# Performance work log

Hardware: AMD Instinct MI355X
Metric: run time of the kernel (lower is better)

## Reference

```python
import jax, jax.numpy as jnp
import numpy as np

LN_EPS = 1e-5
MASK_FILL = -1e10


def setup_inputs() -> dict:
    key = jax.random.key(0)
    ks = jax.random.split(key, 6)
    b, lq, lk, d = 8, 2048, 2048, 256
    q = jax.random.normal(ks[0], (b, lq, d), dtype=jnp.float32)
    k = jax.random.normal(ks[1], (b, lk, d), dtype=jnp.float32)
    v = jax.random.normal(ks[2], (b, lk, d), dtype=jnp.float32)
    # additive-score weight, scaled so logits are O(1)
    shared_attn = jax.random.normal(ks[3], (1, 2 * d), dtype=jnp.float32) / jnp.sqrt(jnp.float32(2 * d))
    fc_w = jax.random.normal(ks[4], (d, d), dtype=jnp.float32) / jnp.sqrt(jnp.float32(d))
    ln_gamma = jnp.ones((d,), dtype=jnp.float32)
    ln_beta = jnp.zeros((d,), dtype=jnp.float32)
    mask = jax.random.randint(ks[5], (b, lq, lk), 0, 2).astype(bool)
    return {"q": q, "k": k, "v": v, "shared_attn": shared_attn,
            "fc_w": fc_w, "ln_gamma": ln_gamma, "ln_beta": ln_beta, "mask": mask}


def reference(q, k, v, shared_attn, fc_w, ln_gamma, ln_beta, mask):
    d_k = q.shape[-1]
    residual = q
    # F.linear(cat([q_exp, k_exp], -1), W) with W:(1, 2*d_k) decomposes as
    # score[b,i,j] = q[b,i] . w_q + k[b,j] . w_k  (rank-1 additive score)
    w_q = shared_attn[0, :d_k]
    w_k = shared_attn[0, d_k:]
    sq = jnp.einsum('bid,d->bi', q, w_q)          # (b, lq)
    sk = jnp.einsum('bjd,d->bj', k, w_k)          # (b, lk)
    attn = sq[:, :, None] + sk[:, None, :]        # (b, lq, lk)
    attn = jnp.where(mask, jnp.float32(MASK_FILL), attn)
    attn = jax.nn.softmax(attn, axis=2)
    out = jnp.einsum('bij,bjd->bid', attn, v)     # (b, lq, d_v)
    out = out @ fc_w.T                            # F.linear(out, fc_w)
    x = out + residual
    mu = jnp.mean(x, axis=-1, keepdims=True)
    var = jnp.var(x, axis=-1, keepdims=True)
    out = (x - mu) / jnp.sqrt(var + LN_EPS) * ln_gamma + ln_beta
    return (out, attn)
```

## Files before the change

### kernel.cpp

```cpp
#include <hip/hip_runtime.h>
#include <hip/hip_bf16.h>

#define BB 8
#define LQ 2048
#define LK 2048
#define DD 256
#define OUT0_N (BB*LQ*DD)

typedef short s16x8 __attribute__((ext_vector_type(8)));
typedef float f32x4 __attribute__((ext_vector_type(4)));

#define GAS __attribute__((address_space(1)))
#define LAS __attribute__((address_space(3)))

__device__ __forceinline__ unsigned short f2b(float x){
  unsigned int u = __float_as_uint(x);
  u += 0x7fffu + ((u >> 16) & 1u);
  return (unsigned short)(u >> 16);
}
__device__ __forceinline__ float b2f(unsigned short h){
  return __uint_as_float(((unsigned int)h) << 16);
}
__device__ __forceinline__ float ldf(const void* p, long i, int bf){
  return bf ? b2f(((const unsigned short*)p)[i]) : ((const float*)p)[i];
}
__device__ __forceinline__ s16x8 ld8(const void* p, long i, int bf){
  if (bf) return *(const s16x8*)((const unsigned short*)p + i);
  const float* f = (const float*)p + i;
  float4 a = *(const float4*)(f);
  float4 c = *(const float4*)(f + 4);
  s16x8 r;
  r[0]=(short)f2b(a.x); r[1]=(short)f2b(a.y); r[2]=(short)f2b(a.z); r[3]=(short)f2b(a.w);
  r[4]=(short)f2b(c.x); r[5]=(short)f2b(c.y); r[6]=(short)f2b(c.z); r[7]=(short)f2b(c.w);
  return r;
}
__device__ __forceinline__ float wsum(float v){
  #pragma unroll
  for (int o=32;o;o>>=1) v += __shfl_xor(v, o, 64);
  return v;
}

__device__ __forceinline__ void detect_flags(const void* q, const void* mask,
                                             int& mbytes, int& bf){
  __shared__ int s_bf, s_mb;
  int t = threadIdx.x;
  if (t == 0){ s_bf = 0; s_mb = 0; }
  __syncthreads();
  if (t < 256){
    float x = fabsf(((const float*)q)[t]);
    if (x > 1e-6f && x < 100.0f) atomicAdd(&s_bf, 1);
    unsigned int mw = ((const unsigned int*)mask)[t];
    if (mw > 1u) atomicOr(&s_mb, 1);
  }
  __syncthreads();
  bf = (s_bf < 128) ? 1 : 0;
  mbytes = s_mb;
}

__global__ __launch_bounds__(256) void k_prep(const void* q, const void* kk,
    const void* v, const void* sh, const void* fc, const void* mask,
    float* e, unsigned short* vtf){
  int mbytes, bf;
  detect_flags(q, mask, mbytes, bf);
  (void)mbytes;
  int lane = threadIdx.x & 63;

  if (blockIdx.x >= 1024){
    int wid = ((blockIdx.x - 1024) << 2) + (threadIdx.x >> 6);
    long base = (long)wid * DD + lane * 4;
    float acc;
    if (bf){
      ushort4 kv = *(const ushort4*)((const unsigned short*)kk + base);
      ushort4 wv = *(const ushort4*)((const unsigned short*)sh + DD + lane*4);
      acc = b2f(kv.x)*b2f(wv.x) + b2f(kv.y)*b2f(wv.y)
          + b2f(kv.z)*b2f(wv.z) + b2f(kv.w)*b2f(wv.w);
    } else {
      float4 kv = *(const float4*)((const float*)kk + base);
      float4 wv = *(const float4*)((const float*)sh + DD + lane*4);
      acc = kv.x*wv.x + kv.y*wv.y + kv.z*wv.z + kv.w*wv.w;
    }
    acc = wsum(acc);
    if (lane == 0) e[wid] = __expf(acc);
    return;
  }

  int wid  = (blockIdx.x << 2) + (threadIdx.x >> 6);
  int dbase = (wid & 15) << 4;
  int jbase = (wid >> 4) << 6;
  int r = lane & 15, g = lane >> 4;
  f32x4 acc[4];
  #pragma unroll
  for (int t2=0;t2<4;t2++) acc[t2] = (f32x4){0.f,0.f,0.f,0.f};
  #pragma unroll
  for (int ks = 0; ks < 8; ++ks){
    int k0 = ks*32 + g*8;
    s16x8 bv = ld8(fc, (long)(dbase + r)*DD + k0, bf);
    #pragma unroll
    for (int t2 = 0; t2 < 4; ++t2){
      s16x8 a = ld8(v, (long)(jbase + t2*16 + r)*DD + k0, bf);
      acc[t2] = __builtin_amdgcn_mfma_f32_16x16x32_bf16(a, bv, acc[t2], 0, 0, 0);
    }
  }
  int b  = jbase >> 11;
  int jj = jbase & 2047;
  int d  = dbase + r;
  #pragma unroll
  for (int t2 = 0; t2 < 4; ++t2){
    int kidx = (jj >> 3) + t2*2 + (g >> 1);
    long idx = ((long)(b*256 + kidx))*2048 + (long)d*8 + (g & 1)*4;
    ushort4 w4;
    w4.x = f2b(acc[t2][0]); w4.y = f2b(acc[t2][1]);
    w4.z = f2b(acc[t2][2]); w4.w = f2b(acc[t2][3]);
    *(ushort4*)(vtf + idx) = w4;
  }
}

__device__ __forceinline__ s16x8 afrag(const unsigned int (*bits_s)[66],
    const unsigned short* e16_s, int row, int kk){
  int w0 = (kk >> 2) & 63;
  int nib4 = (kk >> 8) << 2;
  unsigned lo = (bits_s[row][w0]   >> nib4) & 0xFu;
  unsigned hi = (bits_s[row][w0+1] >> nib4) & 0xFu;
  unsigned m8 = lo | (hi << 4);
  union { s16x8 v; unsigned u[4]; } a;
  a.v = *(const s16x8*)(&e16_s[kk]);
  #pragma unroll
  for (int i = 0; i < 4; ++i){
    unsigned w = a.u[i];
    w = (m8 & (1u << (2*i)))   ? (w & 0xFFFF0000u) : w;
    w = (m8 & (1u << (2*i+1))) ? (w & 0x0000FFFFu) : w;
    a.u[i] = w;
  }
  return a.v;
}

__global__ __launch_bounds__(512, 4) void k_pvf(void* d_out, const unsigned short* vtf,
    const void* q, const void* gamp, const void* betp, const void* mask,
    const float* e){
  __shared__ __align__(16) char smem[80256];
  unsigned int (*bits_s)[66] = reinterpret_cast<unsigned int(*)[66]>(smem + 65536);
  unsigned short* e16_s      = (unsigned short*)(smem + 73984);
  float* scale_s             = (float*)(smem + 78080);
  float* gs                  = (float*)(smem + 78208);
  float* bs                  = (float*)(smem + 79232);
  float* redp                = (float*)smem;
  #define RED(nh_, row_, col_) redp[(((nh_)*32)+(row_))*132 + (col_)]

  int mbytes, bf;
  detect_flags(q, mask, mbytes, bf);
  int o     = ((blockIdx.x & 7) << 6) + (blockIdx.x >> 3);
  int b     = o >> 6;
  int rbase = (o & 63) << 5;
  int t = threadIdx.x, lane = t & 63, wid = t >> 6;
  int nh = wid & 1, ks = wid >> 1;
  int r16 = lane >> 4, c16 = lane & 15;
  int dbase = nh << 7;
  const float* eb = e + b * LK;
  const unsigned short* vtfb = vtf + (long)b * 256 * 2048;
  char* stag = smem + wid * 8192;

  auto STAGE = [&](int j){
    int ss = j >> 1, h = j & 1;
    int k0 = (ks << 9) + (ss << 5);
    const char* g = (const char*)vtfb +
        (((long)((k0 >> 3) + r16) * 256 + dbase + c16) << 4);
    char* lb = stag + (j & 1) * 4096;
    #pragma unroll
    for (int i = 0; i < 4; ++i)
      __builtin_amdgcn_global_load_lds(
        (const GAS unsigned int*)(g + h*1024 + i*256),
        (LAS unsigned int*)(lb + i*1024), 16, 0, 0);
  };

  { float4 ef = ((const float4*)eb)[t];
    ushort4 u; u.x=f2b(ef.x); u.y=f2b(ef.y); u.z=f2b(ef.z); u.w=f2b(ef.w);
    *(ushort4*)(&e16_s[t*4]) = u; }
  if (t < 256){ gs[t] = ldf(gamp, t, bf); bs[t] = ldf(betp, t, bf); }

  unsigned short* attn16 = (unsigned short*)d_out + OUT0_N;
  float*          attn32 = (float*)d_out + OUT0_N;
  #pragma unroll 1
  for (int rr = 0; rr < 4; ++rr){
    int row = (wid << 2) + rr;
    long rowm = ((long)(b*LQ + rbase + row)) * (long)LK;
    unsigned int bw = 0;
    float4 ev[8];
    float s = 0.f;
    #pragma unroll
    for (int w = 0; w < 8; ++w){
      int j = (w << 8) + (lane << 2);
      unsigned int m4;
      if (mbytes){
        unsigned int mb = *(const unsigned int*)((const unsigned char*)mask + rowm + j);
        m4 = (mb & 1u) | ((mb >> 7) & 2u) | ((mb >> 14) & 4u) | ((mb >> 21) & 8u);
      } else {
        int4 mi = *(const int4*)((const int*)mask + rowm + j);
        m4 = (mi.x?1u:0u) | (mi.y?2u:0u) | (mi.z?4u:0u) | (mi.w?8u:0u);
      }
      bw |= m4 << (w*4);
      ev[w] = *(const float4*)(eb + j);
      if (!(m4 & 1u)) s += ev[w].x;
      if (!(m4 & 2u)) s += ev[w].y;
      if (!(m4 & 4u)) s += ev[w].z;
      if (!(m4 & 8u)) s += ev[w].w;
    }
    s = wsum(s);
    float scal = (s > 0.f) ? (1.0f/s) : -1.0f;
    bits_s[row][lane] = bw;
    if (lane == 0) scale_s[row] = scal;
    #pragma unroll
    for (int w = 0; w < 8; ++w){
      int j = (w << 8) + (lane << 2);
      float p0,p1,p2,p3;
      if (scal < 0.f){ p0=p1=p2=p3 = 1.0f/2048.0f; }
      else {
        p0 = (bw >> (w*4  )) & 1u ? 0.f : ev[w].x * scal;
        p1 = (bw >> (w*4+1)) & 1u ? 0.f : ev[w].y * scal;
        p2 = (bw >> (w*4+2)) & 1u ? 0.f : ev[w].z * scal;
        p3 = (bw >> (w*4+3)) & 1u ? 0.f : ev[w].w * scal;
      }
      if (bf){
        ushort4 u4; u4.x=f2b(p0); u4.y=f2b(p1); u4.z=f2b(p2); u4.w=f2b(p3);
        *(ushort4*)(attn16 + rowm + j) = u4;
      } else {
        float4 f4 = {p0,p1,p2,p3};
        *(float4*)(attn32 + rowm + j) = f4;
      }
    }
  }
  STAGE(0); STAGE(1);
  __syncthreads();

  float sc0 = scale_s[c16];
  float sc1 = scale_s[16 + c16];
  s16x8 cf;
  #pragma unroll
  for (int i = 0; i < 8; ++i) cf[i] = (short)0x3A00;

  f32x4 acc[2][8];
  #pragma unroll
  for (int i=0;i<2;i++)
    #pragma unroll
    for (int j=0;j<8;j++) acc[i][j] = (f32x4){0.f,0.f,0.f,0.f};

  #pragma unroll 1
  for (int s = 0; s < 16; ++s){
    int k0 = (ks << 9) + (s << 5);
    s16x8 A0 = (sc0 < 0.f) ? cf : afrag(bits_s, e16_s, c16,      k0 + r16*8);
    s16x8 A1 = (sc1 < 0.f) ? cf : afrag(bits_s, e16_s, 16 + c16, k0 + r16*8);
    #pragma unroll
    for (int h = 0; h < 2; ++h){
      int j = 2*s + h;
      if (j < 31) asm volatile("s_waitcnt vmcnt(4)" ::: "memory");
      else        asm volatile("s_waitcnt vmcnt(0)" ::: "memory");
      __builtin_amdgcn_sched_barrier(0);
      const char* lb = stag + (j & 1) * 4096;
      s16x8 Bv0 = *(const s16x8*)(lb +    0 + (lane << 4));
      s16x8 Bv1 = *(const s16x8*)(lb + 1024 + (lane << 4));
      s16x8 Bv2 = *(const s16x8*)(lb + 2048 + (lane << 4));
      s16x8 Bv3 = *(const s16x8*)(lb + 3072 + (lane << 4));
      __builtin_amdgcn_sched_barrier(0);
      if (j + 2 < 32) STAGE(j + 2);
      acc[0][h*4+0] = __builtin_amdgcn_mfma_f32_16x16x32_bf16(A0, Bv0, acc[0][h*4+0], 0,0,0);
      acc[1][h*4+0] = __builtin_amdgcn_mfma_f32_16x16x32_bf16(A1, Bv0, acc[1][h*4+0], 0,0,0);
      acc[0][h*4+1] = __builtin_amdgcn_mfma_f32_16x16x32_bf16(A0, Bv1, acc[0][h*4+1], 0,0,0);
      acc[1][h*4+1] = __builtin_amdgcn_mfma_f32_16x16x32_bf16(A1, Bv1, acc[1][h*4+1], 0,0,0);
      acc[0][h*4+2] = __builtin_amdgcn_mfma_f32_16x16x32_bf16(A0, Bv2, acc[0][h*4+2], 0,0,0);
      acc[1][h*4+2] = __builtin_amdgcn_mfma_f32_16x16x32_bf16(A1, Bv2, acc[1][h*4+2], 0,0,0);
      acc[0][h*4+3] = __builtin_amdgcn_mfma_f32_16x16x32_bf16(A0, Bv3, acc[0][h*4+3], 0,0,0);
      acc[1][h*4+3] = __builtin_amdgcn_mfma_f32_16x16x32_bf16(A1, Bv3, acc[1][h*4+3], 0,0,0);
    }
  }
  __syncthreads();

  #pragma unroll
  for (int r = 1; r < 4; ++r){
    if (ks == r){
      #pragma unroll
      for (int mi = 0; mi < 2; ++mi)
        #pragma unroll
        for (int ni = 0; ni < 8; ++ni)
          #pragma unroll
          for (int reg = 0; reg < 4; ++reg)
            RED(nh, mi*16 + r16*4 + reg, ni*16 + c16) = acc[mi][ni][reg];
    }
    __syncthreads();
    if (ks == 0){
      #pragma unroll
      for (int mi = 0; mi < 2; ++mi)
        #pragma unroll
        for (int ni = 0; ni < 8; ++ni)
          #pragma unroll
          for (int reg = 0; reg < 4; ++reg)
            acc[mi][ni][reg] += RED(nh, mi*16 + r16*4 + reg, ni*16 + c16);
    }
    __syncthreads();
  }
  if (ks == 0){
    #pragma unroll
    for (int mi = 0; mi < 2; ++mi)
      #pragma unroll
      for (int ni = 0; ni < 8; ++ni)
        #pragma unroll
        for (int reg = 0; reg < 4; ++reg)
          RED(nh, mi*16 + r16*4 + reg, ni*16 + c16) = acc[mi][ni][reg];
  }
  __syncthreads();

  {
    int row = t >> 4, cg = t & 15;
    int nh2 = cg >> 3, coff = (cg & 7) << 4;
    float sc = scale_s[row];
    float sce = (sc < 0.f) ? 1.0f : sc;
    long grow = (long)b*LQ + rbase + row;
    float xv[16];
    float ps = 0.f, pq = 0.f;
    #pragma unroll
    for (int i4 = 0; i4 < 4; ++i4){
      float4 rv = *(const float4*)(&RED(nh2, row, coff + i4*4));
      float rr[4] = {rv.x, rv.y, rv.z, rv.w};
      int col0 = (cg << 4) + i4*4;
      float qv[4];
      if (bf){
        ushort4 qu = *(const ushort4*)((const unsigned short*)q + grow*DD + col0);
        qv[0]=b2f(qu.x); qv[1]=b2f(qu.y); qv[2]=b2f(qu.z); qv[3]=b2f(qu.w);
      } else {
        float4 qf = *(const float4*)((const float*)q + grow*DD + col0);
        qv[0]=qf.x; qv[1]=qf.y; qv[2]=qf.z; qv[3]=qf.w;
      }
      #pragma unroll
      for (int i = 0; i < 4; ++i){
        float x = rr[i]*sce + qv[i];
        xv[i4*4 + i] = x;
        ps += x; pq += x*x;
      }
    }
    ps += __shfl_xor(ps, 1, 64); pq += __shfl_xor(pq, 1, 64);
    ps += __shfl_xor(ps, 2, 64); pq += __shfl_xor(pq, 2, 64);
    ps += __shfl_xor(ps, 4, 64); pq += __shfl_xor(pq, 4, 64);
    ps += __shfl_xor(ps, 8, 64); pq += __shfl_xor(pq, 8, 64);
    float mu = ps * (1.0f/256.0f);
    float var = pq * (1.0f/256.0f) - mu*mu;
    float rs = rsqrtf(var + 1e-5f);
    #pragma unroll
    for (int i4 = 0; i4 < 4; ++i4){
      int col0 = (cg << 4) + i4*4;
      float y[4];
      #pragma unroll
      for (int i = 0; i < 4; ++i){
        int col = col0 + i;
        y[i] = (xv[i4*4 + i] - mu) * rs * gs[col] + bs[col];
      }
      long oi = grow*(long)DD + col0;
      if (bf){
        ushort4 u4; u4.x=f2b(y[0]); u4.y=f2b(y[1]); u4.z=f2b(y[2]); u4.w=f2b(y[3]);
        *(ushort4*)((unsigned short*)d_out + oi) = u4;
      } else {
        float4 f4 = {y[0],y[1],y[2],y[3]};
        *(float4*)((float*)d_out + oi) = f4;
      }
    }
  }
  #undef RED
}

extern "C" void kernel_launch(void* const* d_in, const int* in_sizes, int n_in,
                              void* d_out, int out_size, void* d_ws, size_t ws_size,
                              hipStream_t stream) {
  const void* q    = d_in[0];
  const void* k    = d_in[1];
  const void* v    = d_in[2];
  const void* sh   = d_in[3];
  const void* fc   = d_in[4];
  const void* gam  = d_in[5];
  const void* bet  = d_in[6];
  const void* mask = d_in[7];

  float*          e   = (float*)((char*)d_ws + 65536);
  unsigned short* vtf = (unsigned short*)((char*)d_ws + 4456448);

  k_prep<<<5120, 256, 0, stream>>>(q, k, v, sh, fc, mask, e, vtf);
  k_pvf <<<512,  512, 0, stream>>>(d_out, vtf, q, gam, bet, mask, e);
}
```

Baseline: 128.0 us.

## Split mask/softmax output into separate kernel, feed bitmask and scales to GEMM

Moves the per-row mask reading, softmax normalisation and attention-matrix write out of the fused GEMM kernel into a new k_mask kernel with 4096 small blocks, storing packed mask bits and row scales in workspace. The GEMM kernel now loads those bits and scales, issues its first V stages earlier, and moves the next-stage prefetch after the MFMAs with an explicit lgkmcnt wait. The aim is to spread the bandwidth-heavy attention write across many more blocks instead of 512 large ones, at the cost of an extra launch and a workspace round trip for bits and scales.

```diff
diff --git a/kernel.cpp b/kernel.cpp
--- a/kernel.cpp
+++ b/kernel.cpp
@@ -115,12 +115,68 @@
   }
 }
 
+__global__ __launch_bounds__(256) void k_mask(const void* q, const void* mask,
+    const float* e, void* d_out, unsigned int* bits, float* scale){
+  int mbytes, bf;
+  detect_flags(q, mask, mbytes, bf);
+  int row  = (blockIdx.x << 2) + (threadIdx.x >> 6);
+  int lane = threadIdx.x & 63;
+  int b = row >> 11;
+  const float* eb = e + b * LK;
+  long rowm = (long)row * LK;
+  unsigned int bw = 0;
+  float4 ev[8];
+  float s = 0.f;
+  #pragma unroll
+  for (int w = 0; w < 8; ++w){
+    int j = (w << 8) + (lane << 2);
+    unsigned int m4;
+    if (mbytes){
+      unsigned int mb = *(const unsigned int*)((const unsigned char*)mask + rowm + j);
+      m4 = (mb & 1u) | ((mb >> 7) & 2u) | ((mb >> 14) & 4u) | ((mb >> 21) & 8u);
+    } else {
+      int4 mi = *(const int4*)((const int*)mask + rowm + j);
+      m4 = (mi.x?1u:0u) | (mi.y?2u:0u) | (mi.z?4u:0u) | (mi.w?8u:0u);
+    }
+    bw |= m4 << (w*4);
+    ev[w] = *(const float4*)(eb + j);
+    if (!(m4 & 1u)) s += ev[w].x;
+    if (!(m4 & 2u)) s += ev[w].y;
+    if (!(m4 & 4u)) s += ev[w].z;
+    if (!(m4 & 8u)) s += ev[w].w;
+  }
+  s = wsum(s);
+  float scal = (s > 0.f) ? (1.0f/s) : -1.0f;
+  bits[(long)row*64 + lane] = bw;
+  if (lane == 0) scale[row] = scal;
+  #pragma unroll
+  for (int w = 0; w < 8; ++w){
+    int j = (w << 8) + (lane << 2);
+    float p0,p1,p2,p3;
+    if (scal < 0.f){ p0=p1=p2=p3 = 1.0f/2048.0f; }
+    else {
+      p0 = (bw >> (w*4  )) & 1u ? 0.f : ev[w].x * scal;
+      p1 = (bw >> (w*4+1)) & 1u ? 0.f : ev[w].y * scal;
+      p2 = (bw >> (w*4+2)) & 1u ? 0.f : ev[w].z * scal;
+      p3 = (bw >> (w*4+3)) & 1u ? 0.f : ev[w].w * scal;
+    }
+    if (bf){
+      ushort4 u4; u4.x=f2b(p0); u4.y=f2b(p1); u4.z=f2b(p2); u4.w=f2b(p3);
+      *(ushort4*)((unsigned short*)d_out + OUT0_N + rowm + j) = u4;
+    } else {
+      float4 f4 = {p0,p1,p2,p3};
+      *(float4*)((float*)d_out + OUT0_N + rowm + j) = f4;
+    }
+  }
+}
+
 __device__ __forceinline__ s16x8 afrag(const unsigned int (*bits_s)[66],
     const unsigned short* e16_s, int row, int kk){
   int w0 = (kk >> 2) & 63;
   int nib4 = (kk >> 8) << 2;
-  unsigned lo = (bits_s[row][w0]   >> nib4) & 0xFu;
-  unsigned hi = (bits_s[row][w0+1] >> nib4) & 0xFu;
+  uint2 bw2 = *(const uint2*)(&bits_s[row][w0]);
+  unsigned lo = (bw2.x >> nib4) & 0xFu;
+  unsigned hi = (bw2.y >> nib4) & 0xFu;
   unsigned m8 = lo | (hi << 4);
   union { s16x8 v; unsigned u[4]; } a;
   a.v = *(const s16x8*)(&e16_s[kk]);
@@ -134,9 +190,9 @@
   return a.v;
 }
 
-__global__ __launch_bounds__(512, 4) void k_pvf(void* d_out, const unsigned short* vtf,
+__global__ __launch_bounds__(512, 4) void k_gemm(void* d_out, const unsigned short* vtf,
     const void* q, const void* gamp, const void* betp, const void* mask,
-    const float* e){
+    const unsigned int* bits, const float* e, const float* scaleg){
   __shared__ __align__(16) char smem[80256];
   unsigned int (*bits_s)[66] = reinterpret_cast<unsigned int(*)[66]>(smem + 65536);
   unsigned short* e16_s      = (unsigned short*)(smem + 73984);
@@ -148,6 +204,7 @@
 
   int mbytes, bf;
   detect_flags(q, mask, mbytes, bf);
+  (void)mbytes;
   int o     = ((blockIdx.x & 7) << 6) + (blockIdx.x >> 3);
   int b     = o >> 6;
   int rbase = (o & 63) << 5;
@@ -172,63 +229,17 @@
         (LAS unsigned int*)(lb + i*1024), 16, 0, 0);
   };
 
+  STAGE(0); STAGE(1);
+
   { float4 ef = ((const float4*)eb)[t];
     ushort4 u; u.x=f2b(ef.x); u.y=f2b(ef.y); u.z=f2b(ef.z); u.w=f2b(ef.w);
     *(ushort4*)(&e16_s[t*4]) = u; }
+  { int rr = t >> 4, wq = (t & 15) << 2;
+    uint4 wv = *(const uint4*)(bits + ((long)(b*LQ + rbase + rr))*64 + wq);
+    bits_s[rr][wq+0]=wv.x; bits_s[rr][wq+1]=wv.y;
+    bits_s[rr][wq+2]=wv.z; bits_s[rr][wq+3]=wv.w; }
+  if (t < 32) scale_s[t] = scaleg[(long)b*LQ + rbase + t];
   if (t < 256){ gs[t] = ldf(gamp, t, bf); bs[t] = ldf(betp, t, bf); }
-
-  unsigned short* attn16 = (unsigned short*)d_out + OUT0_N;
-  float*          attn32 = (float*)d_out + OUT0_N;
-  #pragma unroll 1
-  for (int rr = 0; rr < 4; ++rr){
-    int row = (wid << 2) + rr;
-    long rowm = ((long)(b*LQ + rbase + row)) * (long)LK;
-    unsigned int bw = 0;
-    float4 ev[8];
-    float s = 0.f;
-    #pragma unroll
-    for (int w = 0; w < 8; ++w){
-      int j = (w << 8) + (lane << 2);
-      unsigned int m4;
-      if (mbytes){
-        unsigned int mb = *(const unsigned int*)((const unsigned char*)mask + rowm + j);
-        m4 = (mb & 1u) | ((mb >> 7) & 2u) | ((mb >> 14) & 4u) | ((mb >> 21) & 8u);
-      } else {
-        int4 mi = *(const int4*)((const int*)mask + rowm + j);
-        m4 = (mi.x?1u:0u) | (mi.y?2u:0u) | (mi.z?4u:0u) | (mi.w?8u:0u);
-      }
-      bw |= m4 << (w*4);
-      ev[w] = *(const float4*)(eb + j);
-      if (!(m4 & 1u)) s += ev[w].x;
-      if (!(m4 & 2u)) s += ev[w].y;
-      if (!(m4 & 4u)) s += ev[w].z;
-      if (!(m4 & 8u)) s += ev[w].w;
-    }
-    s = wsum(s);
-    float scal = (s > 0.f) ? (1.0f/s) : -1.0f;
-    bits_s[row][lane] = bw;
-    if (lane == 0) scale_s[row] = scal;
-    #pragma unroll
-    for (int w = 0; w < 8; ++w){
-      int j = (w << 8) + (lane << 2);
-      float p0,p1,p2,p3;
-      if (scal < 0.f){ p0=p1=p2=p3 = 1.0f/2048.0f; }
-      else {
-        p0 = (bw >> (w*4  )) & 1u ? 0.f : ev[w].x * scal;
-        p1 = (bw >> (w*4+1)) & 1u ? 0.f : ev[w].y * scal;
-        p2 = (bw >> (w*4+2)) & 1u ? 0.f : ev[w].z * scal;
-        p3 = (bw >> (w*4+3)) & 1u ? 0.f : ev[w].w * scal;
-      }
-      if (bf){
-        ushort4 u4; u4.x=f2b(p0); u4.y=f2b(p1); u4.z=f2b(p2); u4.w=f2b(p3);
-        *(ushort4*)(attn16 + rowm + j) = u4;
-      } else {
-        float4 f4 = {p0,p1,p2,p3};
-        *(float4*)(attn32 + rowm + j) = f4;
-      }
-    }
-  }
-  STAGE(0); STAGE(1);
   __syncthreads();
 
   float sc0 = scale_s[c16];
@@ -253,14 +264,11 @@
       int j = 2*s + h;
       if (j < 31) asm volatile("s_waitcnt vmcnt(4)" ::: "memory");
       else        asm volatile("s_waitcnt vmcnt(0)" ::: "memory");
-      __builtin_amdgcn_sched_barrier(0);
       const char* lb = stag + (j & 1) * 4096;
       s16x8 Bv0 = *(const s16x8*)(lb +    0 + (lane << 4));
       s16x8 Bv1 = *(const s16x8*)(lb + 1024 + (lane << 4));
       s16x8 Bv2 = *(const s16x8*)(lb + 2048 + (lane << 4));
       s16x8 Bv3 = *(const s16x8*)(lb + 3072 + (lane << 4));
-      __builtin_amdgcn_sched_barrier(0);
-      if (j + 2 < 32) STAGE(j + 2);
       acc[0][h*4+0] = __builtin_amdgcn_mfma_f32_16x16x32_bf16(A0, Bv0, acc[0][h*4+0], 0,0,0);
       acc[1][h*4+0] = __builtin_amdgcn_mfma_f32_16x16x32_bf16(A1, Bv0, acc[1][h*4+0], 0,0,0);
       acc[0][h*4+1] = __builtin_amdgcn_mfma_f32_16x16x32_bf16(A0, Bv1, acc[0][h*4+1], 0,0,0);
@@ -269,6 +277,9 @@
       acc[1][h*4+2] = __builtin_amdgcn_mfma_f32_16x16x32_bf16(A1, Bv2, acc[1][h*4+2], 0,0,0);
       acc[0][h*4+3] = __builtin_amdgcn_mfma_f32_16x16x32_bf16(A0, Bv3, acc[0][h*4+3], 0,0,0);
       acc[1][h*4+3] = __builtin_amdgcn_mfma_f32_16x16x32_bf16(A1, Bv3, acc[1][h*4+3], 0,0,0);
+      asm volatile("s_waitcnt lgkmcnt(0)" ::: "memory");
+      __builtin_amdgcn_sched_barrier(0);
+      if (j + 2 < 32) STAGE(j + 2);
     }
   }
   __syncthreads();
@@ -322,8 +333,8 @@
       int col0 = (cg << 4) + i4*4;
       float qv[4];
       if (bf){
-        ushort4 qu = *(const ushort4*)((const unsigned short*)q + grow*DD + col0);
-        qv[0]=b2f(qu.x); qv[1]=b2f(qu.y); qv[2]=b2f(qu.z); qv[3]=b2f(qu.w);
+        const unsigned short* qp = (const unsigned short*)q + grow*DD + col0;
+        qv[0]=b2f(qp[0]); qv[1]=b2f(qp[1]); qv[2]=b2f(qp[2]); qv[3]=b2f(qp[3]);
       } else {
         float4 qf = *(const float4*)((const float*)q + grow*DD + col0);
         qv[0]=qf.x; qv[1]=qf.y; qv[2]=qf.z; qv[3]=qf.w;
@@ -376,9 +387,12 @@
   const void* bet  = d_in[6];
   const void* mask = d_in[7];
 
-  float*          e   = (float*)((char*)d_ws + 65536);
-  unsigned short* vtf = (unsigned short*)((char*)d_ws + 4456448);
+  float*          e     = (float*)((char*)d_ws + 65536);
+  float*          scale = (float*)((char*)d_ws + 131072);
+  unsigned int*   bits  = (unsigned int*)((char*)d_ws + 262144);
+  unsigned short* vtf   = (unsigned short*)((char*)d_ws + 4456448);
 
   k_prep<<<5120, 256, 0, stream>>>(q, k, v, sh, fc, mask, e, vtf);
-  k_pvf <<<512,  512, 0, stream>>>(d_out, vtf, q, gam, bet, mask, e);
-}
+  k_mask<<<4096, 256, 0, stream>>>(q, mask, e, d_out, bits, scale);
+  k_gemm<<<512,  512, 0, stream>>>(d_out, vtf, q, gam, bet, mask, bits, e, scale);
+}
```

Result: slower. 140.3 us (+9.6%).
